# Optimization experiments

Hardware: AMD Instinct MI355X
Metric: run time of the kernel (lower is better)

The kernel has to match this reference:

```python
import jax, jax.numpy as jnp
import numpy as np

B, S, H, NH = 16, 1024, 512, 8
DH = H // NH
EPS = 1e-12
COV_MIN = 1e-24


def _split_heads(x):
    b, s, _ = x.shape
    return x.reshape(b, s, NH, DH).transpose(0, 2, 1, 3)  # [B,NH,S,DH]


def _merge_heads(x):
    b, nh, s, dh = x.shape
    return x.transpose(0, 2, 1, 3).reshape(b, s, nh * dh)


def _layernorm(x, w, b):
    u = jnp.mean(x, -1, keepdims=True)
    s = jnp.mean((x - u) ** 2, -1, keepdims=True)
    return w * ((x - u) / jnp.sqrt(s + EPS)) + b


def _wasserstein(mq, cq, mk, ck):
    # mean part: ||mq_i - mk_j||^2 via matmul expansion
    ret = (-2.0 * jnp.einsum('bhid,bhjd->bhij', mq, mk)
           + jnp.sum(mq ** 2, -1)[..., :, None]
           + jnp.sum(mk ** 2, -1)[..., None, :])
    sq_cq = jnp.sqrt(jnp.clip(cq, COV_MIN))
    sq_ck = jnp.sqrt(jnp.clip(ck, COV_MIN))
    cov_ret = (-2.0 * jnp.einsum('bhid,bhjd->bhij', sq_cq, sq_ck)
               + jnp.sum(cq, -1)[..., :, None]
               + jnp.sum(ck, -1)[..., None, :])
    return ret + cov_ret


def setup_inputs() -> dict:
    key = jax.random.key(0)
    ks = jax.random.split(key, 16)
    d = {
        'x_mean': jax.random.normal(ks[0], (B, S, H), jnp.float32),
        'x_resp_mean': jax.random.normal(ks[1], (B, S, H), jnp.float32),
        'x_cov': jax.random.normal(ks[2], (B, S, H), jnp.float32),
        'x_resp_cov': jax.random.normal(ks[3], (B, S, H), jnp.float32),
    }
    causal = jnp.tril(jnp.ones((S, S), bool))
    d['attn_mask'] = jnp.where(causal, 0.0, -1e4).astype(jnp.float32)[None, None]
    names = ['mq', 'mk', 'mv', 'cq', 'ck', 'cv', 'md', 'cd']
    for i, n in enumerate(names):
        d[n + '_w'] = jax.random.normal(ks[4 + i], (H, H), jnp.float32) * 0.02
        d[n + '_b'] = jnp.zeros((H,), jnp.float32)
    d['ln_w'] = jnp.ones((H,), jnp.float32)
    d['ln_b'] = jnp.zeros((H,), jnp.float32)
    return d


def reference(x_mean, x_resp_mean, x_cov, x_resp_cov, attn_mask,
              mq_w, mq_b, mk_w, mk_b, mv_w, mv_b,
              cq_w, cq_b, ck_w, ck_b, cv_w, cv_b,
              md_w, md_b, cd_w, cd_b, ln_w, ln_b):
    mq = _split_heads(x_mean @ mq_w + mq_b)
    mk = _split_heads(x_mean @ mk_w + mk_b)
    mv = _split_heads(x_resp_mean @ mv_w + mv_b)
    cq = _split_heads(jax.nn.elu(x_cov @ cq_w + cq_b) + 1.0)
    ck = _split_heads(jax.nn.elu(x_cov @ ck_w + ck_b) + 1.0)
    cv = _split_heads(jax.nn.elu(x_resp_cov @ cv_w + cv_b) + 1.0)

    scores = -_wasserstein(mq, cq, mk, ck) / np.sqrt(DH).astype(np.float32)
    scores = scores + attn_mask
    probs = jax.nn.softmax(scores, axis=-1)  # [B,NH,S,S]
    # zero_pad=True: zero out the first query row
    probs = probs.at[:, :, 0, :].set(0.0)

    mean_ctx = _merge_heads(jnp.einsum('bhij,bhjd->bhid', probs, mv))
    cov_ctx = _merge_heads(jnp.einsum('bhij,bhjd->bhid', probs ** 2, cv))

    mean_h = _layernorm(mean_ctx @ md_w + md_b + x_mean, ln_w, ln_b)
    cov_h = _layernorm(cov_ctx @ cd_w + cd_b + x_cov, ln_w, ln_b)
    return mean_h, cov_h, probs
```

## Files before the change

kernel.cpp:

```cpp
#include <hip/hip_runtime.h>
#include <math.h>

#define SLEN 1024
#define NH 8
#define DH 64
#define HDIM 512
#define BATCH 16
#define NROWS (BATCH * SLEN)
#define BHN (BATCH * NH)
#define BHROWS (BHN * SLEN)

typedef short bf16x8 __attribute__((ext_vector_type(8)));
typedef unsigned short u16x8 __attribute__((ext_vector_type(8)));
typedef float f32x4 __attribute__((ext_vector_type(4)));

__device__ __forceinline__ unsigned short f2bf(float f) {
    unsigned u = __float_as_uint(f);
    u += 0x7fffu + ((u >> 16) & 1u);
    return (unsigned short)(u >> 16);
}
__device__ __forceinline__ float bf2f(unsigned short h) {
    return __uint_as_float(((unsigned)h) << 16);
}

struct Args {
    const float *xm, *xrm, *xc, *xrc;
    const float *w[8], *bias[8];
    const float *ln_w, *ln_b;
    unsigned short *xbf, *wt;
    float *sums;
    unsigned short *qcat, *kcat, *vcat, *vcat_t, *ctxm, *ctxc;
    float *out_m, *out_c, *probs;
};

__global__ void __launch_bounds__(256) cvt_inputs_k(Args P) {
    const int which = blockIdx.y;
    const float *s = which == 0 ? P.xm : which == 1 ? P.xrm : which == 2 ? P.xc : P.xrc;
    unsigned short *d = P.xbf + (size_t)which * 8388608;
    const long long i = ((long long)blockIdx.x * 256 + threadIdx.x) * 8;
    if (i >= 8388608) return;
    float4 a = *(const float4 *)(s + i);
    float4 b = *(const float4 *)(s + i + 4);
    u16x8 o;
    o[0] = f2bf(a.x); o[1] = f2bf(a.y); o[2] = f2bf(a.z); o[3] = f2bf(a.w);
    o[4] = f2bf(b.x); o[5] = f2bf(b.y); o[6] = f2bf(b.z); o[7] = f2bf(b.w);
    *(u16x8 *)(d + i) = o;
}

__global__ void __launch_bounds__(256) wtrans_k(Args P) {
    const int op = blockIdx.y;
    const float *W = P.w[op];
    unsigned short *WT = P.wt + (size_t)op * 262144;
    const int kt = blockIdx.x >> 3, nt = blockIdx.x & 7;
    __shared__ float Ws[64][65];
    const int t = threadIdx.x;
#pragma unroll
    for (int it = 0; it < 4; ++it) {
        int g = t + 256 * it;
        int k = g >> 4, n4 = (g & 15) * 4;
        float4 v = *(const float4 *)(W + (size_t)(kt * 64 + k) * 512 + nt * 64 + n4);
        Ws[k][n4] = v.x; Ws[k][n4 + 1] = v.y; Ws[k][n4 + 2] = v.z; Ws[k][n4 + 3] = v.w;
    }
    __syncthreads();
#pragma unroll
    for (int it = 0; it < 2; ++it) {
        int g = t + 256 * it;
        int n = g >> 3, kg = (g & 7) * 8;
        u16x8 o;
#pragma unroll
        for (int e = 0; e < 8; ++e) o[e] = f2bf(Ws[kg + e][n]);
        *(u16x8 *)(WT + (size_t)(nt * 64 + n) * 512 + kt * 64 + kg) = o;
    }
}

__global__ void __launch_bounds__(256) mgemm0_k(Args P) {
    const int op = blockIdx.z;
    const int srcidx[6] = {0, 0, 1, 2, 2, 3};
    const unsigned short *Abf = P.xbf + (size_t)srcidx[op] * 8388608;
    const unsigned short *WT = P.wt + (size_t)op * 262144;
    const float *bias = P.bias[op];
    unsigned short *dstb; int doff, act;
    switch (op) {
        case 0: dstb = P.qcat; doff = 0;  act = 0; break;
        case 1: dstb = P.kcat; doff = 0;  act = 0; break;
        case 2: dstb = P.vcat; doff = 0;  act = 0; break;
        case 3: dstb = P.qcat; doff = 64; act = 1; break;
        case 4: dstb = P.kcat; doff = 64; act = 1; break;
        default:dstb = P.vcat; doff = 64; act = 2; break;
    }
    const int lin = blockIdx.y * 4 + blockIdx.x;
    const int xcd = lin & 7, idx = lin >> 3;
    const int m0 = (xcd * 16 + (idx >> 2)) * 128;
    const int n0 = (idx & 3) * 128;

    __shared__ unsigned short As[128][64];
    __shared__ unsigned short Bs[128][64];
    const int t = threadIdx.x;
    const int wid = t >> 6, lane = t & 63;
    const int wm = wid >> 1, wn = wid & 1;
    const int l16 = lane & 15, lq = lane >> 4;

    f32x4 acc[4][4];
#pragma unroll
    for (int i = 0; i < 4; ++i)
#pragma unroll
        for (int j = 0; j < 4; ++j) acc[i][j] = (f32x4)(0.f);

    for (int k0 = 0; k0 < 512; k0 += 64) {
        __syncthreads();
#pragma unroll
        for (int it = 0; it < 4; ++it) {
            int g = t + 256 * it;
            int r = g >> 3, cg = g & 7;
            bf16x8 av = *(const bf16x8 *)(Abf + (size_t)(m0 + r) * 512 + k0 + cg * 8);
            *(bf16x8 *)&As[r][(cg ^ (r & 7)) * 8] = av;
            bf16x8 bv = *(const bf16x8 *)(WT + (size_t)(n0 + r) * 512 + k0 + cg * 8);
            *(bf16x8 *)&Bs[r][(cg ^ (r & 7)) * 8] = bv;
        }
        __syncthreads();
#pragma unroll
        for (int kk = 0; kk < 2; ++kk) {
            bf16x8 a[4], b[4];
#pragma unroll
            for (int mf = 0; mf < 4; ++mf) {
                int r = wm * 64 + mf * 16 + l16;
                int cg = kk * 4 + lq;
                a[mf] = *(const bf16x8 *)&As[r][(cg ^ (r & 7)) * 8];
            }
#pragma unroll
            for (int nf = 0; nf < 4; ++nf) {
                int r = wn * 64 + nf * 16 + l16;
                int cg = kk * 4 + lq;
                b[nf] = *(const bf16x8 *)&Bs[r][(cg ^ (r & 7)) * 8];
            }
#pragma unroll
            for (int mf = 0; mf < 4; ++mf)
#pragma unroll
                for (int nf = 0; nf < 4; ++nf)
                    acc[mf][nf] = __builtin_amdgcn_mfma_f32_16x16x32_bf16(a[mf], b[nf], acc[mf][nf], 0, 0, 0);
        }
    }

#pragma unroll
    for (int mf = 0; mf < 4; ++mf) {
#pragma unroll
        for (int nf = 0; nf < 4; ++nf) {
#pragma unroll
            for (int r = 0; r < 4; ++r) {
                const int i = m0 + wm * 64 + mf * 16 + lq * 4 + r;
                const int j = n0 + wn * 64 + nf * 16 + l16;
                float v = acc[mf][nf][r] + bias[j];
                if (act == 1) {
                    float e = v > 0.f ? v + 1.f : expf(v);
                    v = sqrtf(fmaxf(e, 1e-24f));
                } else if (act == 2) {
                    v = v > 0.f ? v + 1.f : expf(v);
                }
                const int b_ = i >> 10, s_ = i & (SLEN - 1);
                const int h_ = j >> 6, d_ = j & (DH - 1);
                dstb[((size_t)(b_ * NH + h_) * SLEN + s_) * 128 + doff + d_] = f2bf(v);
            }
        }
    }
}

__global__ void __launch_bounds__(256) vtrans_k(Args P) {
    const int bh = blockIdx.y;
    const int s0 = blockIdx.x * 128;
    __shared__ unsigned short Ts[128][136];
    const unsigned short *src = P.vcat + (size_t)bh * SLEN * 128;
    unsigned short *dst = P.vcat_t + (size_t)bh * 128 * SLEN;
    const int t = threadIdx.x;
#pragma unroll
    for (int it = 0; it < 8; ++it) {
        int g = t + 256 * it;
        int s = g >> 4, dg = g & 15;
        *(u16x8 *)&Ts[s][dg * 8] = *(const u16x8 *)(src + (size_t)(s0 + s) * 128 + dg * 8);
    }
    __syncthreads();
#pragma unroll
    for (int it = 0; it < 8; ++it) {
        int g = t + 256 * it;
        int d = g >> 4, sg = g & 15;
        u16x8 o;
#pragma unroll
        for (int e = 0; e < 8; ++e) o[e] = Ts[sg * 8 + e][d];
        *(u16x8 *)(dst + (size_t)d * SLEN + s0 + sg * 8) = o;
    }
}

__global__ void __launch_bounds__(256) rowsum_k(Args P) {
    const int t = threadIdx.x;
    const int wv = t >> 6, lane = t & 63;
    const long long row = (long long)blockIdx.x * 4 + wv;
    const unsigned short *src = (row < BHROWS) ? P.qcat : P.kcat;
    const long long r = row & (BHROWS - 1);
    const unsigned short *p = src + r * 128;
    float a = bf2f(p[lane]), b = bf2f(p[64 + lane]);
    float v = a * a + b * b;
#pragma unroll
    for (int o = 32; o > 0; o >>= 1) v += __shfl_xor(v, o);
    if (lane == 0) P.sums[row] = v;
}

__global__ void __launch_bounds__(1024, 4) flash_k(Args P) {
    const int bh = blockIdx.x;
    const int qt = 15 - (int)blockIdx.y;
    const int q0 = qt * 64;
    __shared__ unsigned short Ep[64][1024];
    __shared__ unsigned short Ks[64][128];
    __shared__ float Tred[4][64];
    __shared__ float Tsh[64];
    unsigned short (*Vt)[64] = reinterpret_cast<unsigned short (*)[64]>(&Ks[0][0]);

    const int t = threadIdx.x;
    const int w = t >> 6, lane = t & 63;
    const int l16 = lane & 15, lq = lane >> 4;
    const int mg = w >> 2, q4 = w & 3;

    const unsigned short *qc = P.qcat + (size_t)bh * SLEN * 128;
    const unsigned short *kc = P.kcat + (size_t)bh * SLEN * 128;
    const float *qsum = P.sums + (size_t)bh * SLEN;
    const float *ksum = P.sums + BHROWS + (size_t)bh * SLEN;
    float *pout = P.probs + ((size_t)bh * SLEN + q0) * SLEN;

    const unsigned short *qrow = qc + (size_t)(q0 + mg * 16 + l16) * 128;
    bf16x8 qfr[4];
#pragma unroll
    for (int kk = 0; kk < 4; ++kk) qfr[kk] = *(const bf16x8 *)(qrow + (kk * 4 + lq) * 8);
    float qs[4];
#pragma unroll
    for (int r = 0; r < 4; ++r) qs[r] = qsum[q0 + mg * 16 + lq * 4 + r];

    const int nkt = qt + 1;
    float tpart[4] = {0.f, 0.f, 0.f, 0.f};

    const int sr = t >> 4, sg = t & 15;
    const int rK = q4 * 16 + l16;
    bf16x8 kreg = *(const bf16x8 *)(kc + (size_t)sr * 128 + sg * 8);
    float ksreg = ksum[rK];

    for (int kt = 0; kt < nkt; ++kt) {
        __syncthreads();
        *(bf16x8 *)&Ks[sr][(sg ^ (sr & 7)) * 8] = kreg;
        if (kt + 1 < nkt)
            kreg = *(const bf16x8 *)(kc + (size_t)((kt + 1) * 64 + sr) * 128 + sg * 8);
        __syncthreads();

        const float ksv = ksreg;
        if (kt + 1 < nkt) ksreg = ksum[(kt + 1) * 64 + rK];

        f32x4 acc = (f32x4)(0.f);
#pragma unroll
        for (int kk = 0; kk < 4; ++kk) {
            bf16x8 b = *(const bf16x8 *)&Ks[rK][((kk * 4 + lq) ^ (rK & 7)) * 8];
            acc = __builtin_amdgcn_mfma_f32_16x16x32_bf16(qfr[kk], b, acc, 0, 0, 0);
        }
        const int j = kt * 64 + rK;
#pragma unroll
        for (int r = 0; r < 4; ++r) {
            const int row = mg * 16 + lq * 4 + r;
            const int i = q0 + row;
            float sv = (2.f * acc[r] - qs[r] - ksv) * 0.125f;
            float e = (j <= i) ? __expf(sv) : 0.f;
            tpart[r] += e;
            Ep[row][(((j >> 3) ^ (row & 7)) << 3) | (j & 7)] = f2bf(e);
        }
    }

    const int vr = t >> 3, vg = t & 7;
    const unsigned short *vtg = P.vcat_t + (size_t)bh * 128 * SLEN;
    bf16x8 vreg = *(const bf16x8 *)(vtg + (size_t)vr * SLEN + vg * 8);
    {
        const int zrow = t >> 4;
        f32x4 z = (f32x4)(0.f);
        for (int c4 = nkt * 16 + (t & 15); c4 < 256; c4 += 16)
            *(f32x4 *)(pout + (size_t)zrow * SLEN + c4 * 4) = z;
    }

#pragma unroll
    for (int o = 1; o < 16; o <<= 1)
#pragma unroll
        for (int r = 0; r < 4; ++r) tpart[r] += __shfl_xor(tpart[r], o);
    if (l16 == 0) {
#pragma unroll
        for (int r = 0; r < 4; ++r) Tred[q4][mg * 16 + lq * 4 + r] = tpart[r];
    }
    __syncthreads();
    if (t < 64) {
        const int i = q0 + t;
        const float T = Tred[0][t] + Tred[1][t] + Tred[2][t] + Tred[3][t];
        Tsh[t] = (i == 0) ? 0.f : (1.f / T);
    }
    __syncthreads();

    const int cov = q4 >> 1;
    f32x4 pacc[2];
    pacc[0] = (f32x4)(0.f); pacc[1] = (f32x4)(0.f);
    for (int kt = 0; kt < nkt; ++kt) {
        __syncthreads();
        *(bf16x8 *)&Vt[vr][(vg ^ (vr & 7)) * 8] = vreg;
        if (kt + 1 < nkt)
            vreg = *(const bf16x8 *)(vtg + (size_t)vr * SLEN + (kt + 1) * 64 + vg * 8);
        __syncthreads();

#pragma unroll
        for (int kk = 0; kk < 2; ++kk) {
            const int row = mg * 16 + l16;
            const int gg = (kt * 8) + kk * 4 + lq;
            bf16x8 af = *(const bf16x8 *)&Ep[row][((gg ^ (row & 7)) << 3)];
            if (cov) {
                u16x8 u = (u16x8)af, sq;
#pragma unroll
                for (int e = 0; e < 8; ++e) {
                    float f = bf2f(u[e]);
                    sq[e] = f2bf(f * f);
                }
                af = (bf16x8)sq;
            }
#pragma unroll
            for (int nf = 0; nf < 2; ++nf) {
                const int d = q4 * 32 + nf * 16 + l16;
                bf16x8 bf = *(const bf16x8 *)&Vt[d][((kk * 4 + lq) ^ (d & 7)) * 8];
                pacc[nf] = __builtin_amdgcn_mfma_f32_16x16x32_bf16(af, bf, pacc[nf], 0, 0, 0);
            }
        }

        {
            const int prow = t >> 4, slot = t & 15;
            const int col = kt * 64 + slot * 4;
            const int g = col >> 3, o4 = (slot & 1) * 4;
            u16x8 v = *(const u16x8 *)&Ep[prow][((g ^ (prow & 7)) << 3)];
            const float inv = Tsh[prow];
            f32x4 ov;
            if (kt == qt) {
                const int i = q0 + prow;
#pragma unroll
                for (int e = 0; e < 4; ++e)
                    ov[e] = (col + e <= i) ? bf2f(v[o4 + e]) * inv : 0.f;
            } else {
#pragma unroll
                for (int e = 0; e < 4; ++e)
                    ov[e] = bf2f(v[o4 + e]) * inv;
            }
            *(f32x4 *)(pout + (size_t)prow * SLEN + col) = ov;
        }
    }

    unsigned short *dst = cov ? P.ctxc : P.ctxm;
    const int b_ = bh >> 3, h_ = bh & 7;
#pragma unroll
    for (int nf = 0; nf < 2; ++nf) {
#pragma unroll
        for (int r = 0; r < 4; ++r) {
            const int row = mg * 16 + lq * 4 + r;
            const int s_ = q0 + row;
            const float inv = Tsh[row];
            const float scale = cov ? inv * inv : inv;
            dst[((size_t)b_ * SLEN + s_) * HDIM + h_ * 64 + (q4 & 1) * 32 + nf * 16 + l16] =
                f2bf(pacc[nf][r] * scale);
        }
    }
}

__global__ void __launch_bounds__(512, 4) mgemm_ln_k(Args P) {
    const int op = blockIdx.y;
    const unsigned short *Abf = op ? P.ctxc : P.ctxm;
    const unsigned short *WT = P.wt + (size_t)(6 + op) * 262144;
    const float *bias = P.bias[6 + op];
    const float *resid = op ? P.xc : P.xm;
    float *out = op ? P.out_c : P.out_m;
    const int m0 = blockIdx.x * 64;

    __shared__ unsigned short As[64][64];
    __shared__ unsigned short Bs[512][64];
    __shared__ float Red[64][4][2];

    const int t = threadIdx.x;
    const int w = t >> 6, lane = t & 63;
    const int wm = w >> 2, wn = w & 3;
    const int l16 = lane & 15, lq = lane >> 4;

    f32x4 acc[2][8];
#pragma unroll
    for (int mf = 0; mf < 2; ++mf)
#pragma unroll
        for (int nf = 0; nf < 8; ++nf) acc[mf][nf] = (f32x4)(0.f);

    for (int k0 = 0; k0 < 512; k0 += 64) {
        __syncthreads();
        {
            int r = t >> 3, cg = t & 7;
            *(bf16x8 *)&As[r][(cg ^ (r & 7)) * 8] =
                *(const bf16x8 *)(Abf + (size_t)(m0 + r) * 512 + k0 + cg * 8);
        }
#pragma unroll
        for (int it = 0; it < 8; ++it) {
            int g = t + 512 * it;
            int r = g >> 3, cg = g & 7;
            *(bf16x8 *)&Bs[r][(cg ^ (r & 7)) * 8] =
                *(const bf16x8 *)(WT + (size_t)r * 512 + k0 + cg * 8);
        }
        __syncthreads();
#pragma unroll
        for (int kk = 0; kk < 2; ++kk) {
            bf16x8 a[2];
#pragma unroll
            for (int mf = 0; mf < 2; ++mf) {
                int r = wm * 32 + mf * 16 + l16;
                a[mf] = *(const bf16x8 *)&As[r][((kk * 4 + lq) ^ (r & 7)) * 8];
            }
#pragma unroll
            for (int nf = 0; nf < 8; ++nf) {
                int rn = wn * 128 + nf * 16 + l16;
                bf16x8 b = *(const bf16x8 *)&Bs[rn][((kk * 4 + lq) ^ (rn & 7)) * 8];
#pragma unroll
                for (int mf = 0; mf < 2; ++mf)
                    acc[mf][nf] = __builtin_amdgcn_mfma_f32_16x16x32_bf16(a[mf], b, acc[mf][nf], 0, 0, 0);
            }
        }
    }

    float bv[8];
#pragma unroll
    for (int nf = 0; nf < 8; ++nf) bv[nf] = bias[wn * 128 + nf * 16 + l16];

    float s0[2][4], s1[2][4];
#pragma unroll
    for (int mf = 0; mf < 2; ++mf)
#pragma unroll
        for (int r = 0; r < 4; ++r) { s0[mf][r] = 0.f; s1[mf][r] = 0.f; }

#pragma unroll
    for (int mf = 0; mf < 2; ++mf) {
#pragma unroll
        for (int r = 0; r < 4; ++r) {
            const int i = m0 + wm * 32 + mf * 16 + lq * 4 + r;
            const float *rrow = resid + (size_t)i * HDIM + wn * 128 + l16;
#pragma unroll
            for (int nf = 0; nf < 8; ++nf) {
                float x = acc[mf][nf][r] + bv[nf] + rrow[nf * 16];
                acc[mf][nf][r] = x;
                s0[mf][r] += x;
                s1[mf][r] += x * x;
            }
        }
    }
#pragma unroll
    for (int o = 1; o < 16; o <<= 1)
#pragma unroll
        for (int mf = 0; mf < 2; ++mf)
#pragma unroll
            for (int r = 0; r < 4; ++r) {
                s0[mf][r] += __shfl_xor(s0[mf][r], o);
                s1[mf][r] += __shfl_xor(s1[mf][r], o);
            }
    if (l16 == 0) {
#pragma unroll
        for (int mf = 0; mf < 2; ++mf)
#pragma unroll
            for (int r = 0; r < 4; ++r) {
                const int row = wm * 32 + mf * 16 + lq * 4 + r;
                Red[row][wn][0] = s0[mf][r];
                Red[row][wn][1] = s1[mf][r];
            }
    }
    __syncthreads();

    float lnw[8], lnb[8];
#pragma unroll
    for (int nf = 0; nf < 8; ++nf) {
        const int j = wn * 128 + nf * 16 + l16;
        lnw[nf] = P.ln_w[j]; lnb[nf] = P.ln_b[j];
    }
#pragma unroll
    for (int mf = 0; mf < 2; ++mf) {
#pragma unroll
        for (int r = 0; r < 4; ++r) {
            const int row = wm * 32 + mf * 16 + lq * 4 + r;
            const int i = m0 + row;
            const float S  = Red[row][0][0] + Red[row][1][0] + Red[row][2][0] + Red[row][3][0];
            const float SS = Red[row][0][1] + Red[row][1][1] + Red[row][2][1] + Red[row][3][1];
            const float mean = S * (1.f / 512.f);
            const float var = SS * (1.f / 512.f) - mean * mean;
            const float inv = 1.f / sqrtf(var + 1e-12f);
            float *orow = out + (size_t)i * HDIM + wn * 128 + l16;
#pragma unroll
            for (int nf = 0; nf < 8; ++nf)
                orow[nf * 16] = lnw[nf] * ((acc[mf][nf][r] - mean) * inv) + lnb[nf];
        }
    }
}

extern "C" void kernel_launch(void *const *d_in, const int *in_sizes, int n_in,
                              void *d_out, int out_size, void *d_ws, size_t ws_size,
                              hipStream_t stream) {
    (void)in_sizes; (void)n_in; (void)out_size; (void)ws_size;
    Args P;
    P.xm  = (const float *)d_in[0];
    P.xrm = (const float *)d_in[1];
    P.xc  = (const float *)d_in[2];
    P.xrc = (const float *)d_in[3];
    for (int i = 0; i < 8; ++i) {
        P.w[i]    = (const float *)d_in[5 + 2 * i];
        P.bias[i] = (const float *)d_in[6 + 2 * i];
    }
    P.ln_w = (const float *)d_in[21];
    P.ln_b = (const float *)d_in[22];

    char *ws = (char *)d_ws;
    P.xbf    = (unsigned short *)(ws);
    P.vcat_t = (unsigned short *)(ws);
    P.ctxm   = (unsigned short *)(ws + 33554432);
    P.ctxc   = (unsigned short *)(ws + 50331648);
    P.wt     = (unsigned short *)(ws + 67108864);
    P.sums   = (float *)(ws + 71303168);
    P.qcat   = (unsigned short *)(ws + 72351744);
    P.kcat   = (unsigned short *)(ws + 105906176);
    P.vcat   = (unsigned short *)(ws + 139460608);

    P.out_m = (float *)d_out;
    P.out_c = (float *)d_out + 8388608;
    P.probs = (float *)d_out + 16777216;

    cvt_inputs_k<<<dim3(4096, 4), dim3(256), 0, stream>>>(P);
    wtrans_k<<<dim3(64, 8), dim3(256), 0, stream>>>(P);
    mgemm0_k<<<dim3(4, 128, 6), dim3(256), 0, stream>>>(P);
    vtrans_k<<<dim3(8, 128), dim3(256), 0, stream>>>(P);
    rowsum_k<<<dim3(65536), dim3(256), 0, stream>>>(P);
    flash_k<<<dim3(128, 16), dim3(1024), 0, stream>>>(P);
    mgemm_ln_k<<<dim3(256, 2), dim3(512), 0, stream>>>(P);
}
```

Before: 485.2 us.

## Halve flash kernel query tile to 32 rows with 512-thread blocks

The attention kernel now processes 32 query rows per block with 512 threads instead of 64 rows with 1024 threads, doubling the grid. Each thread loads two K and V rows per tile, and the row-sum reduction reuses the K shared buffer instead of separate arrays, shrinking LDS use. The intent is better occupancy and finer load balance across the causal triangle. The cost is that K/V tiles of 64 keys are loaded twice as often per head, and the last tile does extra masked work for half-tile query blocks.

```diff
diff --git a/kernel.cpp b/kernel.cpp
--- a/kernel.cpp
+++ b/kernel.cpp
@@ -203,15 +203,14 @@
     if (lane == 0) P.sums[row] = v;
 }
 
-__global__ void __launch_bounds__(1024, 4) flash_k(Args P) {
+__global__ void __launch_bounds__(512, 4) flash_k(Args P) {
     const int bh = blockIdx.x;
-    const int qt = 15 - (int)blockIdx.y;
-    const int q0 = qt * 64;
-    __shared__ unsigned short Ep[64][1024];
+    const int qt = 31 - (int)blockIdx.y;
+    const int q0 = qt * 32;
+    __shared__ unsigned short Ep[32][1024];
     __shared__ unsigned short Ks[64][128];
-    __shared__ float Tred[4][64];
-    __shared__ float Tsh[64];
     unsigned short (*Vt)[64] = reinterpret_cast<unsigned short (*)[64]>(&Ks[0][0]);
+    float *scr = reinterpret_cast<float *>(&Ks[0][0]);
 
     const int t = threadIdx.x;
     const int w = t >> 6, lane = t & 63;
@@ -232,19 +231,24 @@
 #pragma unroll
     for (int r = 0; r < 4; ++r) qs[r] = qsum[q0 + mg * 16 + lq * 4 + r];
 
-    const int nkt = qt + 1;
+    const int nkt = (q0 >> 6) + 1;
+    const int rK = q4 * 16 + l16;
     float tpart[4] = {0.f, 0.f, 0.f, 0.f};
 
-    const int sr = t >> 4, sg = t & 15;
-    const int rK = q4 * 16 + l16;
-    bf16x8 kreg = *(const bf16x8 *)(kc + (size_t)sr * 128 + sg * 8);
+    const int sr0 = t >> 4, sg = t & 15;
+    const int sr1 = sr0 + 32;
+    bf16x8 kreg0 = *(const bf16x8 *)(kc + (size_t)sr0 * 128 + sg * 8);
+    bf16x8 kreg1 = *(const bf16x8 *)(kc + (size_t)sr1 * 128 + sg * 8);
     float ksreg = ksum[rK];
 
     for (int kt = 0; kt < nkt; ++kt) {
         __syncthreads();
-        *(bf16x8 *)&Ks[sr][(sg ^ (sr & 7)) * 8] = kreg;
-        if (kt + 1 < nkt)
-            kreg = *(const bf16x8 *)(kc + (size_t)((kt + 1) * 64 + sr) * 128 + sg * 8);
+        *(bf16x8 *)&Ks[sr0][(sg ^ (sr0 & 7)) * 8] = kreg0;
+        *(bf16x8 *)&Ks[sr1][(sg ^ (sr1 & 7)) * 8] = kreg1;
+        if (kt + 1 < nkt) {
+            kreg0 = *(const bf16x8 *)(kc + (size_t)((kt + 1) * 64 + sr0) * 128 + sg * 8);
+            kreg1 = *(const bf16x8 *)(kc + (size_t)((kt + 1) * 64 + sr1) * 128 + sg * 8);
+        }
         __syncthreads();
 
         const float ksv = ksreg;
@@ -268,9 +272,6 @@
         }
     }
 
-    const int vr = t >> 3, vg = t & 7;
-    const unsigned short *vtg = P.vcat_t + (size_t)bh * 128 * SLEN;
-    bf16x8 vreg = *(const bf16x8 *)(vtg + (size_t)vr * SLEN + vg * 8);
     {
         const int zrow = t >> 4;
         f32x4 z = (f32x4)(0.f);
@@ -282,26 +283,44 @@
     for (int o = 1; o < 16; o <<= 1)
 #pragma unroll
         for (int r = 0; r < 4; ++r) tpart[r] += __shfl_xor(tpart[r], o);
+    __syncthreads();
     if (l16 == 0) {
 #pragma unroll
-        for (int r = 0; r < 4; ++r) Tred[q4][mg * 16 + lq * 4 + r] = tpart[r];
+        for (int r = 0; r < 4; ++r) scr[q4 * 32 + mg * 16 + lq * 4 + r] = tpart[r];
     }
     __syncthreads();
-    if (t < 64) {
-        const int i = q0 + t;
-        const float T = Tred[0][t] + Tred[1][t] + Tred[2][t] + Tred[3][t];
-        Tsh[t] = (i == 0) ? 0.f : (1.f / T);
+    float invP;
+    {
+        const int row = t >> 4;
+        const float T = scr[row] + scr[32 + row] + scr[64 + row] + scr[96 + row];
+        invP = (q0 + row == 0) ? 0.f : (1.f / T);
+    }
+    float invC[4];
+#pragma unroll
+    for (int r = 0; r < 4; ++r) {
+        const int row = mg * 16 + lq * 4 + r;
+        const float T = scr[row] + scr[32 + row] + scr[64 + row] + scr[96 + row];
+        invC[r] = (q0 + row == 0) ? 0.f : (1.f / T);
     }
     __syncthreads();
 
     const int cov = q4 >> 1;
     f32x4 pacc[2];
     pacc[0] = (f32x4)(0.f); pacc[1] = (f32x4)(0.f);
+    const unsigned short *vtg = P.vcat_t + (size_t)bh * 128 * SLEN;
+    const int vr0 = t >> 3, vg = t & 7;
+    const int vr1 = vr0 + 64;
+    bf16x8 vreg0 = *(const bf16x8 *)(vtg + (size_t)vr0 * SLEN + vg * 8);
+    bf16x8 vreg1 = *(const bf16x8 *)(vtg + (size_t)vr1 * SLEN + vg * 8);
+
     for (int kt = 0; kt < nkt; ++kt) {
         __syncthreads();
-        *(bf16x8 *)&Vt[vr][(vg ^ (vr & 7)) * 8] = vreg;
-        if (kt + 1 < nkt)
-            vreg = *(const bf16x8 *)(vtg + (size_t)vr * SLEN + (kt + 1) * 64 + vg * 8);
+        *(bf16x8 *)&Vt[vr0][(vg ^ (vr0 & 7)) * 8] = vreg0;
+        *(bf16x8 *)&Vt[vr1][(vg ^ (vr1 & 7)) * 8] = vreg1;
+        if (kt + 1 < nkt) {
+            vreg0 = *(const bf16x8 *)(vtg + (size_t)vr0 * SLEN + (kt + 1) * 64 + vg * 8);
+            vreg1 = *(const bf16x8 *)(vtg + (size_t)vr1 * SLEN + (kt + 1) * 64 + vg * 8);
+        }
         __syncthreads();
 
 #pragma unroll
@@ -331,17 +350,16 @@
             const int col = kt * 64 + slot * 4;
             const int g = col >> 3, o4 = (slot & 1) * 4;
             u16x8 v = *(const u16x8 *)&Ep[prow][((g ^ (prow & 7)) << 3)];
-            const float inv = Tsh[prow];
             f32x4 ov;
-            if (kt == qt) {
+            if (kt == nkt - 1) {
                 const int i = q0 + prow;
 #pragma unroll
                 for (int e = 0; e < 4; ++e)
-                    ov[e] = (col + e <= i) ? bf2f(v[o4 + e]) * inv : 0.f;
+                    ov[e] = (col + e <= i) ? bf2f(v[o4 + e]) * invP : 0.f;
             } else {
 #pragma unroll
                 for (int e = 0; e < 4; ++e)
-                    ov[e] = bf2f(v[o4 + e]) * inv;
+                    ov[e] = bf2f(v[o4 + e]) * invP;
             }
             *(f32x4 *)(pout + (size_t)prow * SLEN + col) = ov;
         }
@@ -355,8 +373,7 @@
         for (int r = 0; r < 4; ++r) {
             const int row = mg * 16 + lq * 4 + r;
             const int s_ = q0 + row;
-            const float inv = Tsh[row];
-            const float scale = cov ? inv * inv : inv;
+            const float scale = cov ? invC[r] * invC[r] : invC[r];
             dst[((size_t)b_ * SLEN + s_) * HDIM + h_ * 64 + (q4 & 1) * 32 + nf * 16 + l16] =
                 f2bf(pacc[nf][r] * scale);
         }
@@ -528,6 +545,6 @@
     mgemm0_k<<<dim3(4, 128, 6), dim3(256), 0, stream>>>(P);
     vtrans_k<<<dim3(8, 128), dim3(256), 0, stream>>>(P);
     rowsum_k<<<dim3(65536), dim3(256), 0, stream>>>(P);
-    flash_k<<<dim3(128, 16), dim3(1024), 0, stream>>>(P);
+    flash_k<<<dim3(128, 32), dim3(512), 0, stream>>>(P);
     mgemm_ln_k<<<dim3(256, 2), dim3(512), 0, stream>>>(P);
 }
```

New measurement: 479.3 us (median of 2 runs). No clear change (-1.2%).
